# Kernel optimization log

Hardware: AMD Instinct MI355X
Metric: run time of the kernel (lower is better)

## Reference

```python
import jax, jax.numpy as jnp
import numpy as np

D_MODEL = 1024
NHEAD = 16
HEAD_DIM = D_MODEL // NHEAD


def setup_inputs() -> dict:
    key = jax.random.key(0)
    k1, k2, k3 = jax.random.split(key, 3)
    x = jax.random.normal(k1, (4, 2048, D_MODEL), dtype=jnp.float32)
    # xavier_uniform init for weights, zero bias
    lim_qkv = float(np.sqrt(6.0 / (D_MODEL + 3 * D_MODEL)))
    w_qkv = jax.random.uniform(k2, (3 * D_MODEL, D_MODEL), jnp.float32, -lim_qkv, lim_qkv)
    b_qkv = jnp.zeros((3 * D_MODEL,), jnp.float32)
    lim_o = float(np.sqrt(6.0 / (D_MODEL + D_MODEL)))
    w_o = jax.random.uniform(k3, (D_MODEL, D_MODEL), jnp.float32, -lim_o, lim_o)
    b_o = jnp.zeros((D_MODEL,), jnp.float32)
    return {"x": x, "w_qkv": w_qkv, "b_qkv": b_qkv, "w_o": w_o, "b_o": b_o}


def reference(x, w_qkv, b_qkv, w_o, b_o):
    B, S, _ = x.shape
    qkv = x @ w_qkv.T + b_qkv                      # [B,S,3D]
    qkv = qkv.reshape(B, S, NHEAD, 3 * HEAD_DIM).transpose(0, 2, 1, 3)  # [B,H,S,3d]
    q, k, v = jnp.split(qkv, 3, axis=-1)           # each [B,H,S,d]
    scale = 1.0 / jnp.sqrt(jnp.asarray(HEAD_DIM, x.dtype))
    logits = jnp.einsum('bhqd,bhkd->bhqk', q, k) * scale
    attn = jax.nn.softmax(logits, axis=-1)
    vals = jnp.einsum('bhqk,bhkd->bhqd', attn, v)  # [B,H,S,d]
    vals = vals.transpose(0, 2, 1, 3).reshape(B, S, D_MODEL)
    return vals @ w_o.T + b_o
```

## Files before the change

kernel.cpp:

```cpp
#include <hip/hip_runtime.h>
#include <hip/hip_bf16.h>
#include <stdint.h>

typedef unsigned short u16;
typedef uint32_t u32;
typedef __bf16 bf16x8 __attribute__((ext_vector_type(8)));
typedef float f32x4 __attribute__((ext_vector_type(4)));
typedef float f32x16 __attribute__((ext_vector_type(16)));
typedef u16 u16x4v __attribute__((ext_vector_type(4)));
typedef u32 u32x2 __attribute__((ext_vector_type(2)));

#define AS1 __attribute__((address_space(1)))
#define AS3 __attribute__((address_space(3)))

__device__ __forceinline__ void gld_lds16(const u16* g, u16* l) {
    __builtin_amdgcn_global_load_lds((const AS1 uint32_t*)g, (AS3 uint32_t*)l, 16, 0, 0);
}

__device__ __forceinline__ u16 f2bf(float f) {
    union { float f; uint32_t u; } v; v.f = f;
    uint32_t u = v.u;
    return (u16)((u + 0x7FFFu + ((u >> 16) & 1u)) >> 16);
}

__device__ __forceinline__ u32x2 pl32swap(u32 a, u32 b) {
#if __has_builtin(__builtin_amdgcn_permlane32_swap)
    return __builtin_amdgcn_permlane32_swap(a, b, false, false);
#else
    asm volatile("v_permlane32_swap_b32 %0, %1" : "+v"(a), "+v"(b));
    u32x2 r; r[0] = a; r[1] = b; return r;
#endif
}

#define QSCALE 0.18033688011112042f

__global__ void cast_f32_bf16(const float* __restrict__ in, u16* __restrict__ out, int n4) {
    int i = blockIdx.x * blockDim.x + threadIdx.x;
    if (i < n4) {
        float4 f = ((const float4*)in)[i];
        u16x4v o;
        o.x = f2bf(f.x); o.y = f2bf(f.y); o.z = f2bf(f.z); o.w = f2bf(f.w);
        ((u16x4v*)out)[i] = o;
    }
}

template <int MODE>
__global__ __launch_bounds__(256, 2) void gemm_bt(
    const u16* __restrict__ A, const u16* __restrict__ B,
    const float* __restrict__ bias, float* __restrict__ Cf,
    u16* __restrict__ qb, u16* __restrict__ kb, u16* __restrict__ vT,
    int K, int ldc)
{
    __shared__ __align__(16) u16 As[128 * 32];
    __shared__ __align__(16) u16 Bs[128 * 32];
    const int tid = threadIdx.x;
    const int lane = tid & 63;
    const int w = tid >> 6;
    const int wm = (w >> 1) << 6;
    const int wn = (w & 1) << 6;
    const int r = lane & 15;
    const int q = lane >> 4;

    const int nwgx = gridDim.x;
    const int flat = blockIdx.y * nwgx + blockIdx.x;
    const int cpx = (nwgx * gridDim.y) >> 3;
    const int swz = (flat & 7) * cpx + (flat >> 3);
    const int m0 = (swz / nwgx) << 7;
    const int n0 = (swz % nwgx) << 7;

    const f32x4 zero4 = {0.f, 0.f, 0.f, 0.f};
    f32x4 acc[4][4];
#pragma unroll
    for (int i = 0; i < 4; ++i)
#pragma unroll
        for (int j = 0; j < 4; ++j) acc[i][j] = zero4;

    const int nk = K >> 5;
    for (int kt = 0; kt < nk; ++kt) {
        const int kk = kt << 5;
#pragma unroll
        for (int p = 0; p < 2; ++p) {
            const int idx = (p << 8) + tid;
            const int row = idx >> 2;
            const int cg = ((idx & 3) - (row >> 1)) & 3;
            gld_lds16(A + (m0 + row) * K + kk + (cg << 3), &As[idx << 3]);
            gld_lds16(B + (n0 + row) * K + kk + (cg << 3), &Bs[idx << 3]);
        }
        __syncthreads();
        bf16x8 af[4], bf[4];
#pragma unroll
        for (int i = 0; i < 4; ++i) {
            const int ra = wm + (i << 4) + r;
            af[i] = *(const bf16x8*)&As[((ra << 2) + ((q + (ra >> 1)) & 3)) << 3];
            const int rb = wn + (i << 4) + r;
            bf[i] = *(const bf16x8*)&Bs[((rb << 2) + ((q + (rb >> 1)) & 3)) << 3];
        }
#pragma unroll
        for (int i = 0; i < 4; ++i)
#pragma unroll
            for (int j = 0; j < 4; ++j)
                acc[i][j] = __builtin_amdgcn_mfma_f32_16x16x32_bf16(af[i], bf[j], acc[i][j], 0, 0, 0);
        __syncthreads();
    }

#pragma unroll
    for (int j = 0; j < 4; ++j) {
        const int col = n0 + wn + (j << 4) + r;
        const float bv = bias[col];
        if (MODE == 0) {
#pragma unroll
            for (int i = 0; i < 4; ++i)
#pragma unroll
                for (int ii = 0; ii < 4; ++ii) {
                    const int rowg = m0 + wm + (i << 4) + (q << 2) + ii;
                    Cf[rowg * ldc + col] = acc[i][j][ii] + bv;
                }
        } else {
            const int c0 = n0 + wn + (j << 4);
            const int h = c0 / 192;
            const int rem = c0 - h * 192;
            const int region = rem >> 6;
            const int colp = (h << 6) + (rem - (region << 6)) + r;
            if (region == 0) {
#pragma unroll
                for (int i = 0; i < 4; ++i)
#pragma unroll
                    for (int ii = 0; ii < 4; ++ii) {
                        const int rowg = m0 + wm + (i << 4) + (q << 2) + ii;
                        qb[rowg * 1024 + colp] = f2bf((acc[i][j][ii] + bv) * QSCALE);
                    }
            } else if (region == 1) {
#pragma unroll
                for (int i = 0; i < 4; ++i)
#pragma unroll
                    for (int ii = 0; ii < 4; ++ii) {
                        const int rowg = m0 + wm + (i << 4) + (q << 2) + ii;
                        kb[rowg * 1024 + colp] = f2bf(acc[i][j][ii] + bv);
                    }
            } else {
#pragma unroll
                for (int i = 0; i < 4; ++i) {
                    const int rowg0 = m0 + wm + (i << 4) + (q << 2);
                    u16x4v vv;
                    vv.x = f2bf(acc[i][j][0] + bv);
                    vv.y = f2bf(acc[i][j][1] + bv);
                    vv.z = f2bf(acc[i][j][2] + bv);
                    vv.w = f2bf(acc[i][j][3] + bv);
                    *(u16x4v*)&vT[(size_t)colp * 8192 + rowg0] = vv;
                }
            }
        }
    }
}

__global__ __launch_bounds__(256, 3) void attn(
    const u16* __restrict__ qb, const u16* __restrict__ kb,
    const u16* __restrict__ vT, u16* __restrict__ vals)
{
    __shared__ __align__(16) u16 S[16384];

    const int tid  = threadIdx.x;
    const int lane = tid & 63;
    const int w    = tid >> 6;
    const int c    = lane & 31;
    const int h2   = lane >> 5;
    const int head = blockIdx.x;
    const int q0   = blockIdx.y << 7;
    const int b    = blockIdx.z;
    const size_t rowbase = (size_t)b * 2048;

#pragma unroll
    for (int p = 0; p < 4; ++p) {
        const int idx = (p << 8) + tid;
        const int row = idx >> 3;
        const int cg  = ((idx & 7) - row) & 7;
        gld_lds16(qb + (rowbase + q0 + row) * 1024 + (head << 6) + (cg << 3), &S[idx << 3]);
    }

    const int srow8 = tid >> 3;
    const int scg   = ((tid & 7) - srow8) & 7;
    const u16* gK = kb + (rowbase + srow8) * 1024 + (head << 6) + (scg << 3);
    const u16* gV = vT + (size_t)((head << 6) + srow8) * 8192 + rowbase + (scg << 3);

    {
        u16* buf = S + 8192;
        gld_lds16(gK,             &buf[tid << 3]);
        gld_lds16(gK + 32 * 1024, &buf[2048 + (tid << 3)]);
        gld_lds16(gV,             &buf[4096 + (tid << 3)]);
        gld_lds16(gV + 32 * 8192, &buf[6144 + (tid << 3)]);
    }
    __syncthreads();

    const int qrow = (w << 5) + c;
    bf16x8 bq[4];
#pragma unroll
    for (int dc = 0; dc < 4; ++dc)
        bq[dc] = *(const bf16x8*)&S[(qrow << 6) + ((((dc << 1) + h2 + qrow) & 7) << 3)];
    __syncthreads();

    int aF[4];
#pragma unroll
    for (int i = 0; i < 4; ++i)
        aF[i] = (c << 6) + ((((i << 1) + h2 + c) & 7) << 3);

    f32x16 oacc[2], lacc;
#pragma unroll
    for (int i = 0; i < 16; ++i) { oacc[0][i] = 0.f; oacc[1][i] = 0.f; lacc[i] = 0.f; }

    union { u16 u[8]; bf16x8 v; } Ou;
#pragma unroll
    for (int i = 0; i < 8; ++i) Ou.u[i] = 0x3F80;
    const bf16x8 ones8 = Ou.v;

    const u16* gKr = gK + 65536;
    const u16* gVr = gV + 64;

    for (int kt = 0; kt < 32; ++kt) {
        const int cur = kt & 1;
        if (kt > 0) __syncthreads();
        u16* bufP = (cur == 0) ? (S + 0) : (S + 8192);
        const u16* bufC = (cur == 0) ? (S + 8192) : (S + 0);
        if (kt < 31) {
            gld_lds16(gKr,             &bufP[tid << 3]);
            gld_lds16(gKr + 32 * 1024, &bufP[2048 + (tid << 3)]);
            gld_lds16(gVr,             &bufP[4096 + (tid << 3)]);
            gld_lds16(gVr + 32 * 8192, &bufP[6144 + (tid << 3)]);
            gKr += 65536;
            gVr += 64;
        }
        const u16* Ks  = bufC;
        const u16* VTs = bufC + 4096;

        f32x16 sacc[2];
#pragma unroll
        for (int i = 0; i < 16; ++i) { sacc[0][i] = 0.f; sacc[1][i] = 0.f; }
        __builtin_amdgcn_s_setprio(1);
#pragma unroll
        for (int mt = 0; mt < 2; ++mt)
#pragma unroll
            for (int dc = 0; dc < 4; ++dc) {
                const bf16x8 ak = *(const bf16x8*)&Ks[aF[dc] + (mt << 11)];
                sacc[mt] = __builtin_amdgcn_mfma_f32_32x32x16_bf16(ak, bq[dc], sacc[mt], 0, 0, 0);
            }
        __builtin_amdgcn_s_setprio(0);

#pragma unroll
        for (int mt = 0; mt < 2; ++mt) {
            bf16x8 av[4];
#pragma unroll
            for (int ht = 0; ht < 2; ++ht)
#pragma unroll
                for (int c16 = 0; c16 < 2; ++c16)
                    av[(ht << 1) | c16] =
                        *(const bf16x8*)&VTs[aF[(mt << 1) | c16] + (ht << 11)];

            u32 pk[8];
#pragma unroll
            for (int p = 0; p < 8; ++p) {
                const float e0 = __builtin_amdgcn_exp2f(sacc[mt][2 * p]);
                const float e1 = __builtin_amdgcn_exp2f(sacc[mt][2 * p + 1]);
                union { __hip_bfloat162 h; u32 d; } u;
                u.h = __float22bfloat162_rn(float2{e0, e1});
                pk[p] = u.d;
            }
            const u32x2 r02 = pl32swap(pk[0], pk[2]);
            const u32x2 r13 = pl32swap(pk[1], pk[3]);
            const u32x2 r46 = pl32swap(pk[4], pk[6]);
            const u32x2 r57 = pl32swap(pk[5], pk[7]);
            union { u32 d[4]; bf16x8 v; } A0, A1;
            A0.d[0] = r02[0]; A0.d[1] = r13[0]; A0.d[2] = r02[1]; A0.d[3] = r13[1];
            A1.d[0] = r46[0]; A1.d[1] = r57[0]; A1.d[2] = r46[1]; A1.d[3] = r57[1];

            __builtin_amdgcn_s_setprio(1);
            lacc = __builtin_amdgcn_mfma_f32_32x32x16_bf16(ones8, A0.v, lacc, 0, 0, 0);
            lacc = __builtin_amdgcn_mfma_f32_32x32x16_bf16(ones8, A1.v, lacc, 0, 0, 0);
#pragma unroll
            for (int ht = 0; ht < 2; ++ht) {
                oacc[ht] = __builtin_amdgcn_mfma_f32_32x32x16_bf16(av[(ht << 1) | 0], A0.v, oacc[ht], 0, 0, 0);
                oacc[ht] = __builtin_amdgcn_mfma_f32_32x32x16_bf16(av[(ht << 1) | 1], A1.v, oacc[ht], 0, 0, 0);
            }
            __builtin_amdgcn_s_setprio(0);
        }
    }

    const float inv = 1.f / lacc[0];
    const size_t orow = rowbase + q0 + (w << 5) + c;
#pragma unroll
    for (int ht = 0; ht < 2; ++ht)
#pragma unroll
        for (int r4 = 0; r4 < 4; ++r4) {
            u16x4v vv;
            vv.x = f2bf(oacc[ht][4 * r4 + 0] * inv);
            vv.y = f2bf(oacc[ht][4 * r4 + 1] * inv);
            vv.z = f2bf(oacc[ht][4 * r4 + 2] * inv);
            vv.w = f2bf(oacc[ht][4 * r4 + 3] * inv);
            const int hd0 = (ht << 5) + (r4 << 3) + (h2 << 2);
            *(u16x4v*)&vals[orow * 1024 + (head << 6) + hd0] = vv;
        }
}

extern "C" void kernel_launch(void* const* d_in, const int* in_sizes, int n_in,
                              void* d_out, int out_size, void* d_ws, size_t ws_size,
                              hipStream_t stream) {
    (void)in_sizes; (void)n_in; (void)out_size; (void)ws_size;
    const float* x     = (const float*)d_in[0];
    const float* w_qkv = (const float*)d_in[1];
    const float* b_qkv = (const float*)d_in[2];
    const float* w_o   = (const float*)d_in[3];
    const float* b_o   = (const float*)d_in[4];
    float* out = (float*)d_out;

    char* ws = (char*)d_ws;
    u16* xb    = (u16*)(ws);
    u16* wqkvb = (u16*)(ws + (size_t)(16 << 20));
    u16* wob   = (u16*)(ws + (size_t)(22 << 20));
    u16* qb    = (u16*)(ws + (size_t)(24 << 20));
    u16* kb    = (u16*)(ws + (size_t)(40 << 20));
    u16* vTb   = (u16*)(ws + (size_t)(56 << 20));
    u16* valsb = (u16*)(ws + (size_t)(72 << 20));

    cast_f32_bf16<<<8192, 256, 0, stream>>>(x, xb, 2097152);
    cast_f32_bf16<<<3072, 256, 0, stream>>>(w_qkv, wqkvb, 786432);
    cast_f32_bf16<<<1024, 256, 0, stream>>>(w_o, wob, 262144);

    gemm_bt<1><<<dim3(24, 64), 256, 0, stream>>>(xb, wqkvb, b_qkv, nullptr,
                                                 qb, kb, vTb, 1024, 3072);

    attn<<<dim3(16, 16, 4), 256, 0, stream>>>(qb, kb, vTb, valsb);

    gemm_bt<0><<<dim3(8, 64), 256, 0, stream>>>(valsb, wob, b_o, out,
                                                nullptr, nullptr, nullptr, 1024, 1024);
}
```

Baseline: 292.2 us.

## Double query rows per attention block to reuse K/V tiles across two tiles

Each attention block now handles 256 query rows instead of 128, with each wave holding two 32-row query fragments that share every K and V fragment read from LDS. This halves the global K/V traffic per query and the number of LDS K/V reads per MFMA. In exchange it needs more accumulator registers, so launch bounds drop to 2 blocks per CU and the grid shrinks to 512 blocks, which lowers occupancy and parallelism.

```diff
diff --git a/kernel.cpp b/kernel.cpp
--- a/kernel.cpp
+++ b/kernel.cpp
@@ -153,7 +153,7 @@
     }
 }
 
-__global__ __launch_bounds__(256, 3) void attn(
+__global__ __launch_bounds__(256, 2) void attn(
     const u16* __restrict__ qb, const u16* __restrict__ kb,
     const u16* __restrict__ vT, u16* __restrict__ vals)
 {
@@ -165,17 +165,28 @@
     const int c    = lane & 31;
     const int h2   = lane >> 5;
     const int head = blockIdx.x;
-    const int q0   = blockIdx.y << 7;
+    const int q0   = blockIdx.y << 8;
     const int b    = blockIdx.z;
     const size_t rowbase = (size_t)b * 2048;
 
 #pragma unroll
-    for (int p = 0; p < 4; ++p) {
+    for (int p = 0; p < 8; ++p) {
         const int idx = (p << 8) + tid;
         const int row = idx >> 3;
         const int cg  = ((idx & 7) - row) & 7;
         gld_lds16(qb + (rowbase + q0 + row) * 1024 + (head << 6) + (cg << 3), &S[idx << 3]);
     }
+    __syncthreads();
+
+    bf16x8 bq[4][2];
+#pragma unroll
+    for (int nt = 0; nt < 2; ++nt) {
+        const int qr = (w << 6) + (nt << 5) + c;
+#pragma unroll
+        for (int dc = 0; dc < 4; ++dc)
+            bq[dc][nt] = *(const bf16x8*)&S[(qr << 6) + ((((dc << 1) + h2 + qr) & 7) << 3)];
+    }
+    __syncthreads();
 
     const int srow8 = tid >> 3;
     const int scg   = ((tid & 7) - srow8) & 7;
@@ -191,21 +202,18 @@
     }
     __syncthreads();
 
-    const int qrow = (w << 5) + c;
-    bf16x8 bq[4];
-#pragma unroll
-    for (int dc = 0; dc < 4; ++dc)
-        bq[dc] = *(const bf16x8*)&S[(qrow << 6) + ((((dc << 1) + h2 + qrow) & 7) << 3)];
-    __syncthreads();
-
     int aF[4];
 #pragma unroll
     for (int i = 0; i < 4; ++i)
         aF[i] = (c << 6) + ((((i << 1) + h2 + c) & 7) << 3);
 
-    f32x16 oacc[2], lacc;
-#pragma unroll
-    for (int i = 0; i < 16; ++i) { oacc[0][i] = 0.f; oacc[1][i] = 0.f; lacc[i] = 0.f; }
+    f32x16 oacc[2][2], lacc[2];
+#pragma unroll
+    for (int i = 0; i < 16; ++i) {
+        oacc[0][0][i] = 0.f; oacc[0][1][i] = 0.f;
+        oacc[1][0][i] = 0.f; oacc[1][1][i] = 0.f;
+        lacc[0][i] = 0.f;    lacc[1][i] = 0.f;
+    }
 
     union { u16 u[8]; bf16x8 v; } Ou;
 #pragma unroll
@@ -231,21 +239,20 @@
         const u16* Ks  = bufC;
         const u16* VTs = bufC + 4096;
 
-        f32x16 sacc[2];
-#pragma unroll
-        for (int i = 0; i < 16; ++i) { sacc[0][i] = 0.f; sacc[1][i] = 0.f; }
-        __builtin_amdgcn_s_setprio(1);
-#pragma unroll
-        for (int mt = 0; mt < 2; ++mt)
+#pragma unroll
+        for (int mt = 0; mt < 2; ++mt) {
+            f32x16 s0, s1;
+#pragma unroll
+            for (int i = 0; i < 16; ++i) { s0[i] = 0.f; s1[i] = 0.f; }
+            __builtin_amdgcn_s_setprio(1);
 #pragma unroll
             for (int dc = 0; dc < 4; ++dc) {
                 const bf16x8 ak = *(const bf16x8*)&Ks[aF[dc] + (mt << 11)];
-                sacc[mt] = __builtin_amdgcn_mfma_f32_32x32x16_bf16(ak, bq[dc], sacc[mt], 0, 0, 0);
+                s0 = __builtin_amdgcn_mfma_f32_32x32x16_bf16(ak, bq[dc][0], s0, 0, 0, 0);
+                s1 = __builtin_amdgcn_mfma_f32_32x32x16_bf16(ak, bq[dc][1], s1, 0, 0, 0);
             }
-        __builtin_amdgcn_s_setprio(0);
-
-#pragma unroll
-        for (int mt = 0; mt < 2; ++mt) {
+            __builtin_amdgcn_s_setprio(0);
+
             bf16x8 av[4];
 #pragma unroll
             for (int ht = 0; ht < 2; ++ht)
@@ -254,49 +261,56 @@
                     av[(ht << 1) | c16] =
                         *(const bf16x8*)&VTs[aF[(mt << 1) | c16] + (ht << 11)];
 
-            u32 pk[8];
-#pragma unroll
-            for (int p = 0; p < 8; ++p) {
-                const float e0 = __builtin_amdgcn_exp2f(sacc[mt][2 * p]);
-                const float e1 = __builtin_amdgcn_exp2f(sacc[mt][2 * p + 1]);
-                union { __hip_bfloat162 h; u32 d; } u;
-                u.h = __float22bfloat162_rn(float2{e0, e1});
-                pk[p] = u.d;
+#pragma unroll
+            for (int nt = 0; nt < 2; ++nt) {
+                const f32x16& sv = (nt == 0) ? s0 : s1;
+                u32 pk[8];
+#pragma unroll
+                for (int p = 0; p < 8; ++p) {
+                    const float e0 = __builtin_amdgcn_exp2f(sv[2 * p]);
+                    const float e1 = __builtin_amdgcn_exp2f(sv[2 * p + 1]);
+                    union { __hip_bfloat162 h; u32 d; } u;
+                    u.h = __float22bfloat162_rn(float2{e0, e1});
+                    pk[p] = u.d;
+                }
+                const u32x2 r02 = pl32swap(pk[0], pk[2]);
+                const u32x2 r13 = pl32swap(pk[1], pk[3]);
+                const u32x2 r46 = pl32swap(pk[4], pk[6]);
+                const u32x2 r57 = pl32swap(pk[5], pk[7]);
+                union { u32 d[4]; bf16x8 v; } A0, A1;
+                A0.d[0] = r02[0]; A0.d[1] = r13[0]; A0.d[2] = r02[1]; A0.d[3] = r13[1];
+                A1.d[0] = r46[0]; A1.d[1] = r57[0]; A1.d[2] = r46[1]; A1.d[3] = r57[1];
+
+                __builtin_amdgcn_s_setprio(1);
+                lacc[nt] = __builtin_amdgcn_mfma_f32_32x32x16_bf16(ones8, A0.v, lacc[nt], 0, 0, 0);
+                lacc[nt] = __builtin_amdgcn_mfma_f32_32x32x16_bf16(ones8, A1.v, lacc[nt], 0, 0, 0);
+#pragma unroll
+                for (int ht = 0; ht < 2; ++ht) {
+                    oacc[ht][nt] = __builtin_amdgcn_mfma_f32_32x32x16_bf16(av[(ht << 1) | 0], A0.v, oacc[ht][nt], 0, 0, 0);
+                    oacc[ht][nt] = __builtin_amdgcn_mfma_f32_32x32x16_bf16(av[(ht << 1) | 1], A1.v, oacc[ht][nt], 0, 0, 0);
+                }
+                __builtin_amdgcn_s_setprio(0);
             }
-            const u32x2 r02 = pl32swap(pk[0], pk[2]);
-            const u32x2 r13 = pl32swap(pk[1], pk[3]);
-            const u32x2 r46 = pl32swap(pk[4], pk[6]);
-            const u32x2 r57 = pl32swap(pk[5], pk[7]);
-            union { u32 d[4]; bf16x8 v; } A0, A1;
-            A0.d[0] = r02[0]; A0.d[1] = r13[0]; A0.d[2] = r02[1]; A0.d[3] = r13[1];
-            A1.d[0] = r46[0]; A1.d[1] = r57[0]; A1.d[2] = r46[1]; A1.d[3] = r57[1];
-
-            __builtin_amdgcn_s_setprio(1);
-            lacc = __builtin_amdgcn_mfma_f32_32x32x16_bf16(ones8, A0.v, lacc, 0, 0, 0);
-            lacc = __builtin_amdgcn_mfma_f32_32x32x16_bf16(ones8, A1.v, lacc, 0, 0, 0);
-#pragma unroll
-            for (int ht = 0; ht < 2; ++ht) {
-                oacc[ht] = __builtin_amdgcn_mfma_f32_32x32x16_bf16(av[(ht << 1) | 0], A0.v, oacc[ht], 0, 0, 0);
-                oacc[ht] = __builtin_amdgcn_mfma_f32_32x32x16_bf16(av[(ht << 1) | 1], A1.v, oacc[ht], 0, 0, 0);
+        }
+    }
+
+#pragma unroll
+    for (int nt = 0; nt < 2; ++nt) {
+        const float inv = 1.f / lacc[nt][0];
+        const size_t orow = rowbase + q0 + (w << 6) + (nt << 5) + c;
+#pragma unroll
+        for (int ht = 0; ht < 2; ++ht)
+#pragma unroll
+            for (int r4 = 0; r4 < 4; ++r4) {
+                u16x4v vv;
+                vv.x = f2bf(oacc[ht][nt][4 * r4 + 0] * inv);
+                vv.y = f2bf(oacc[ht][nt][4 * r4 + 1] * inv);
+                vv.z = f2bf(oacc[ht][nt][4 * r4 + 2] * inv);
+                vv.w = f2bf(oacc[ht][nt][4 * r4 + 3] * inv);
+                const int hd0 = (ht << 5) + (r4 << 3) + (h2 << 2);
+                *(u16x4v*)&vals[orow * 1024 + (head << 6) + hd0] = vv;
             }
-            __builtin_amdgcn_s_setprio(0);
-        }
-    }
-
-    const float inv = 1.f / lacc[0];
-    const size_t orow = rowbase + q0 + (w << 5) + c;
-#pragma unroll
-    for (int ht = 0; ht < 2; ++ht)
-#pragma unroll
-        for (int r4 = 0; r4 < 4; ++r4) {
-            u16x4v vv;
-            vv.x = f2bf(oacc[ht][4 * r4 + 0] * inv);
-            vv.y = f2bf(oacc[ht][4 * r4 + 1] * inv);
-            vv.z = f2bf(oacc[ht][4 * r4 + 2] * inv);
-            vv.w = f2bf(oacc[ht][4 * r4 + 3] * inv);
-            const int hd0 = (ht << 5) + (r4 << 3) + (h2 << 2);
-            *(u16x4v*)&vals[orow * 1024 + (head << 6) + hd0] = vv;
-        }
+    }
 }
 
 extern "C" void kernel_launch(void* const* d_in, const int* in_sizes, int n_in,
@@ -326,7 +340,7 @@
     gemm_bt<1><<<dim3(24, 64), 256, 0, stream>>>(xb, wqkvb, b_qkv, nullptr,
                                                  qb, kb, vTb, 1024, 3072);
 
-    attn<<<dim3(16, 16, 4), 256, 0, stream>>>(qb, kb, vTb, valsb);
+    attn<<<dim3(16, 8, 4), 256, 0, stream>>>(qb, kb, vTb, valsb);
 
     gemm_bt<0><<<dim3(8, 64), 256, 0, stream>>>(valsb, wob, b_o, out,
                                                 nullptr, nullptr, nullptr, 1024, 1024);
```

New measurement: 276.4 us. 5.4% less time.
